# Kernel tuning notes

Hardware: AMD Instinct MI355X
Metric: run time of the kernel (lower is better)

Reference implementation:

```python
import jax, jax.numpy as jnp
import numpy as np

N, E, D = 50000, 1600000, 32
P = 2.0  # exponent self.p


def setup_inputs() -> dict:
    key = jax.random.key(0)
    k1, k2, k3 = jax.random.split(key, 3)
    X = jax.random.normal(k1, (N, D), dtype=jnp.float32)
    edge_index = jax.random.randint(k2, (2, E), 0, N)
    W = jax.random.normal(k3, (D, D), dtype=jnp.float32) / np.float32(np.sqrt(D))
    b = jnp.zeros((D,), dtype=jnp.float32)
    return {"X": X, "edge_index": edge_index, "W": W, "b": b}


def gcn_conv(X, edge_index, W, b, n):
    # PyG GCNConv: add self-loops, symmetric deg^-1/2 normalization,
    # aggregate messages from source col -> target row.
    src, dst = edge_index[0], edge_index[1]
    loops = jnp.arange(n)
    row = jnp.concatenate([dst, loops])  # targets
    col = jnp.concatenate([src, loops])  # sources
    deg = jax.ops.segment_sum(jnp.ones(row.shape, X.dtype), row, num_segments=n)
    dinv = jax.lax.rsqrt(jnp.maximum(deg, 1.0))  # deg >= 1 (self-loops)
    h = X @ W  # [N, D]
    msg = h[col] * (dinv[col] * dinv[row])[:, None]  # [E+N, D]
    return jax.ops.segment_sum(msg, row, num_segments=n) + b


def reference(X, edge_index, W, b):
    n = X.shape[0]
    h = jax.nn.relu(gcn_conv(X, edge_index, W, b, n))  # activation(conv(X, ei))
    src, dst = edge_index[0], edge_index[1]
    e = jnp.abs(h[src] - h[dst]) ** P  # [E, D] gather + pow
    s = jax.ops.segment_sum(e, src, num_segments=n)  # scatter-sum by source
    cnt = jax.ops.segment_sum(jnp.ones((e.shape[0],), h.dtype), src, num_segments=n)
    mean = s / jnp.maximum(cnt, 1.0)[:, None]  # scatter-mean finalize
    return jnp.tanh(mean)
```

## Files before the change

### kernel.cpp

```cpp
#include <hip/hip_runtime.h>

#define D 32
#define CSH 7
#define KMASK 127
#define PSH 23
#define PMASK ((1u << PSH) - 1u)
#define NBMAX 512

typedef unsigned int uint;

__device__ inline uint bf16rne(float f) {
    uint u = __float_as_uint(f);
    return (u + 0x7FFFu + ((u >> 16) & 1u)) >> 16;
}
__device__ inline float bf_lo(uint w) { return __uint_as_float(w << 16); }
__device__ inline float bf_hi(uint w) { return __uint_as_float(w & 0xFFFF0000u); }
__device__ inline uint bf_pack(float x, float y) { return bf16rne(x) | (bf16rne(y) << 16); }

__global__ void zero_kernel(int* __restrict__ p, int n) {
    int i = threadIdx.x;
    if (i < n) p[i] = 0;
}

__global__ void __launch_bounds__(1024)
coarse_scatter(const int* __restrict__ src, const int* __restrict__ dst,
               int* __restrict__ gCurD, int* __restrict__ gCurS,
               uint* __restrict__ coarseD, uint* __restrict__ coarseS,
               int E, int cap) {
    __shared__ uint stageD[4096], stageS[4096];
    __shared__ int hD[NBMAX], hS[NBMAX];
    __shared__ int preD[NBMAX], preS[NBMAX];
    __shared__ int offD[NBMAX + 1], offS[NBMAX + 1];
    __shared__ int baseD[NBMAX], baseS[NBMAX];
    int t = threadIdx.x;
    if (t < NBMAX) { hD[t] = 0; hS[t] = 0; }
    __syncthreads();
    int s[4], d[4], lpD[4], lpS[4];
    int j0 = blockIdx.x * 4096 + 4 * t;
    int nv = 0;
    if (j0 + 3 < E) {
        int4 s4 = *(const int4*)(src + j0);
        int4 d4 = *(const int4*)(dst + j0);
        s[0] = s4.x; s[1] = s4.y; s[2] = s4.z; s[3] = s4.w;
        d[0] = d4.x; d[1] = d4.y; d[2] = d4.z; d[3] = d4.w;
        nv = 4;
    } else {
        for (int u = 0; u < 4; ++u) {
            int j = j0 + u;
            if (j < E) { s[nv] = src[j]; d[nv] = dst[j]; ++nv; }
        }
    }
    for (int u = 0; u < nv; ++u) {
        lpD[u] = atomicAdd(&hD[d[u] >> CSH], 1);
        lpS[u] = atomicAdd(&hS[s[u] >> CSH], 1);
    }
    __syncthreads();
    {
        int l = t & (NBMAX - 1);
        int* h    = (t < NBMAX) ? hD : hS;
        int* pre  = (t < NBMAX) ? preD : preS;
        int* off  = (t < NBMAX) ? offD : offS;
        int* base = (t < NBMAX) ? baseD : baseS;
        int* gC   = (t < NBMAX) ? gCurD : gCurS;
        pre[l] = h[l];
        __syncthreads();
        for (int stp = 1; stp < NBMAX; stp <<= 1) {
            int x = (l >= stp) ? pre[l - stp] : 0;
            __syncthreads();
            pre[l] += x;
            __syncthreads();
        }
        off[l] = pre[l] - h[l];
        if (l == NBMAX - 1) off[NBMAX] = pre[l];
        if (h[l]) base[l] = atomicAdd(&gC[l], h[l]);
    }
    __syncthreads();
    for (int u = 0; u < nv; ++u) {
        stageD[offD[d[u] >> CSH] + lpD[u]] = ((uint)(d[u] & KMASK) << PSH) | (uint)s[u];
        stageS[offS[s[u] >> CSH] + lpS[u]] = ((uint)(s[u] & KMASK) << PSH) | (uint)d[u];
    }
    __syncthreads();
    int totD = offD[NBMAX];
    for (int j = t; j < totD; j += 1024) {
        int lo = 0, hi = NBMAX;
        while (hi - lo > 1) { int mid = (lo + hi) >> 1; if (offD[mid] <= j) lo = mid; else hi = mid; }
        int rel = baseD[lo] + (j - offD[lo]);
        if (rel < cap) coarseD[(size_t)lo * cap + rel] = stageD[j];
    }
    int totS = offS[NBMAX];
    for (int j = t; j < totS; j += 1024) {
        int lo = 0, hi = NBMAX;
        while (hi - lo > 1) { int mid = (lo + hi) >> 1; if (offS[mid] <= j) lo = mid; else hi = mid; }
        int rel = baseS[lo] + (j - offS[lo]);
        if (rel < cap) coarseS[(size_t)lo * cap + rel] = stageS[j];
    }
}

__global__ void deg_dinv_kernel(const uint* __restrict__ coarseD, const int* __restrict__ gCurD,
                                float* __restrict__ dinv, int N, int cap) {
    __shared__ int cnt[128];
    int b = blockIdx.x, t = threadIdx.x;
    if (t < 128) cnt[t] = 0;
    __syncthreads();
    size_t lo = (size_t)b * cap;
    int n = min(gCurD[b], cap - 512);
    int n4 = n >> 2;
    const uint4* c4 = (const uint4*)(coarseD + lo);
    for (int kk = t; kk < n4; kk += 1024) {
        uint4 e4 = c4[kk];
        atomicAdd(&cnt[e4.x >> PSH], 1);
        atomicAdd(&cnt[e4.y >> PSH], 1);
        atomicAdd(&cnt[e4.z >> PSH], 1);
        atomicAdd(&cnt[e4.w >> PSH], 1);
    }
    for (int kk = 4 * n4 + t; kk < n; kk += 1024)
        atomicAdd(&cnt[coarseD[lo + kk] >> PSH], 1);
    __syncthreads();
    int node = (b << CSH) + t;
    if (t < 128 && node < N) dinv[node] = rsqrtf((float)(cnt[t] + 1));
}

__global__ void matmul_scale_kernel(const float* __restrict__ X, const float* __restrict__ W,
                                    const float* __restrict__ dinv, uint* __restrict__ hs16,
                                    int N) {
    __shared__ float Wl[D * D];
    __shared__ float Xl[8 * D];
    int tid = threadIdx.x;
    for (int k = tid; k < D * D; k += 256) Wl[k] = W[k];
    int row0 = blockIdx.x * 8;
    int g = row0 * D + tid;
    Xl[tid] = (g < N * D) ? X[g] : 0.f;
    __syncthreads();
    int r = tid >> 5;
    int d = tid & 31;
    int row = row0 + r;
    float acc = 0.f;
    #pragma unroll
    for (int k = 0; k < D; ++k) acc += Xl[r * D + k] * Wl[k * D + d];
    if (row < N) acc *= dinv[row];
    float other = __shfl_xor(acc, 1);
    if (row < N && (d & 1) == 0)
        hs16[row * 16 + (d >> 1)] = bf_pack(acc, other);
}

__global__ void __launch_bounds__(1024)
conv_fused(const uint* __restrict__ coarseD, const int* __restrict__ gCurD,
           const uint* __restrict__ hs16, const float* __restrict__ bias,
           uint* __restrict__ h2_16, int N, int cap) {
    extern __shared__ uint adjL[];
    __shared__ int cnt[128];
    __shared__ int pre[128];
    __shared__ int rs[128];
    __shared__ int degL[128];
    int b = blockIdx.x;
    int t = threadIdx.x;
    int nodeLo = b << CSH;
    int nNodes = min(128, N - nodeLo);
    if (t < 128) cnt[t] = 0;
    __syncthreads();
    size_t lo = (size_t)b * cap;
    int n = min(gCurD[b], cap - 512);
    int n4 = n >> 2;
    const uint4* c4 = (const uint4*)(coarseD + lo);
    for (int kk = t; kk < n4; kk += 1024) {
        uint4 e4 = c4[kk];
        atomicAdd(&cnt[e4.x >> PSH], 1);
        atomicAdd(&cnt[e4.y >> PSH], 1);
        atomicAdd(&cnt[e4.z >> PSH], 1);
        atomicAdd(&cnt[e4.w >> PSH], 1);
    }
    for (int kk = 4 * n4 + t; kk < n; kk += 1024)
        atomicAdd(&cnt[coarseD[lo + kk] >> PSH], 1);
    __syncthreads();
    int mydeg = 0, mypad = 0;
    if (t < 128) { mydeg = cnt[t]; mypad = (mydeg + 3) & ~3; pre[t] = mypad; }
    __syncthreads();
    for (int off = 1; off < 128; off <<= 1) {
        int x = 0;
        if (t < 128 && t >= off) x = pre[t - off];
        __syncthreads();
        if (t < 128) pre[t] += x;
        __syncthreads();
    }
    if (t < 128) {
        rs[t] = pre[t] - mypad;
        degL[t] = mydeg;
        cnt[t] = pre[t] - mypad;
    }
    __syncthreads();
    for (int kk = t; kk < n; kk += 1024) {
        uint e = coarseD[lo + kk];
        int pos = atomicAdd(&cnt[e >> PSH], 1);
        if (pos < cap) adjL[pos] = e & PMASK;
    }
    __syncthreads();
    int wave = t >> 6, lane = t & 63;
    int p = lane & 15, slot = lane >> 4;
    for (int nl = wave; nl < nNodes; nl += 16) {
        int s = rs[nl];
        int e = s + degL[nl];
        float ax0 = 0.f, ay0 = 0.f, ax1 = 0.f, ay1 = 0.f;
        float ax2 = 0.f, ay2 = 0.f, ax3 = 0.f, ay3 = 0.f;
        int k = s;
        for (; k + 15 < e; k += 16) {
            uint4 iv = *(const uint4*)(adjL + k + slot * 4);
            uint w0 = hs16[iv.x * 16 + p];
            uint w1 = hs16[iv.y * 16 + p];
            uint w2 = hs16[iv.z * 16 + p];
            uint w3 = hs16[iv.w * 16 + p];
            ax0 += bf_lo(w0); ay0 += bf_hi(w0);
            ax1 += bf_lo(w1); ay1 += bf_hi(w1);
            ax2 += bf_lo(w2); ay2 += bf_hi(w2);
            ax3 += bf_lo(w3); ay3 += bf_hi(w3);
        }
        for (; k < e; k += 4) {
            int kk = k + slot;
            if (kk < e) {
                uint w = hs16[adjL[kk] * 16 + p];
                ax0 += bf_lo(w); ay0 += bf_hi(w);
            }
        }
        float accx = (ax0 + ax1) + (ax2 + ax3);
        float accy = (ay0 + ay1) + (ay2 + ay3);
        accx += __shfl_xor(accx, 16); accy += __shfl_xor(accy, 16);
        accx += __shfl_xor(accx, 32); accy += __shfl_xor(accy, 32);
        if (slot == 0) {
            int node = nodeLo + nl;
            uint wself = hs16[(size_t)node * 16 + p];
            float di = rsqrtf((float)(degL[nl] + 1));
            float vx = di * (accx + bf_lo(wself)) + bias[2 * p];
            float vy = di * (accy + bf_hi(wself)) + bias[2 * p + 1];
            h2_16[(size_t)node * 16 + p] = bf_pack(fmaxf(vx, 0.f), fmaxf(vy, 0.f));
        }
    }
}

__global__ void __launch_bounds__(1024)
pow_fused(const uint* __restrict__ coarseS, const int* __restrict__ gCurS,
          const uint* __restrict__ h2_16, float* __restrict__ out, int N, int cap) {
    extern __shared__ uint adjL[];
    __shared__ int cnt[128];
    __shared__ int pre[128];
    __shared__ int rs[128];
    __shared__ int degL[128];
    __shared__ uint self[128 * 16];
    int b = blockIdx.x;
    int t = threadIdx.x;
    int nodeLo = b << CSH;
    int nNodes = min(128, N - nodeLo);
    if (t < 128) cnt[t] = 0;
    for (int i = t; i < nNodes * 16; i += 1024)
        self[i] = h2_16[(size_t)(nodeLo + (i >> 4)) * 16 + (i & 15)];
    __syncthreads();
    size_t lo = (size_t)b * cap;
    int n = min(gCurS[b], cap - 512);
    int n4 = n >> 2;
    const uint4* c4 = (const uint4*)(coarseS + lo);
    for (int kk = t; kk < n4; kk += 1024) {
        uint4 e4 = c4[kk];
        atomicAdd(&cnt[e4.x >> PSH], 1);
        atomicAdd(&cnt[e4.y >> PSH], 1);
        atomicAdd(&cnt[e4.z >> PSH], 1);
        atomicAdd(&cnt[e4.w >> PSH], 1);
    }
    for (int kk = 4 * n4 + t; kk < n; kk += 1024)
        atomicAdd(&cnt[coarseS[lo + kk] >> PSH], 1);
    __syncthreads();
    int mydeg = 0, mypad = 0;
    if (t < 128) { mydeg = cnt[t]; mypad = (mydeg + 3) & ~3; pre[t] = mypad; }
    __syncthreads();
    for (int off = 1; off < 128; off <<= 1) {
        int x = 0;
        if (t < 128 && t >= off) x = pre[t - off];
        __syncthreads();
        if (t < 128) pre[t] += x;
        __syncthreads();
    }
    if (t < 128) {
        rs[t] = pre[t] - mypad;
        degL[t] = mydeg;
        cnt[t] = pre[t] - mypad;
    }
    __syncthreads();
    for (int kk = t; kk < n; kk += 1024) {
        uint e = coarseS[lo + kk];
        int pos = atomicAdd(&cnt[e >> PSH], 1);
        if (pos < cap) adjL[pos] = e & PMASK;
    }
    __syncthreads();
    int wave = t >> 6, lane = t & 63;
    int p = lane & 15, slot = lane >> 4;
    for (int nl = wave; nl < nNodes; nl += 16) {
        int s = rs[nl];
        int e = s + degL[nl];
        uint wh = self[nl * 16 + p];
        float hx = bf_lo(wh), hy = bf_hi(wh);
        float ax0 = 0.f, ay0 = 0.f, ax1 = 0.f, ay1 = 0.f;
        float ax2 = 0.f, ay2 = 0.f, ax3 = 0.f, ay3 = 0.f;
        int k = s;
        for (; k + 15 < e; k += 16) {
            uint4 iv = *(const uint4*)(adjL + k + slot * 4);
            uint w0 = h2_16[iv.x * 16 + p];
            uint w1 = h2_16[iv.y * 16 + p];
            uint w2 = h2_16[iv.z * 16 + p];
            uint w3 = h2_16[iv.w * 16 + p];
            float vx0 = hx - bf_lo(w0), vy0 = hy - bf_hi(w0);
            float vx1 = hx - bf_lo(w1), vy1 = hy - bf_hi(w1);
            float vx2 = hx - bf_lo(w2), vy2 = hy - bf_hi(w2);
            float vx3 = hx - bf_lo(w3), vy3 = hy - bf_hi(w3);
            ax0 += vx0 * vx0; ay0 += vy0 * vy0;
            ax1 += vx1 * vx1; ay1 += vy1 * vy1;
            ax2 += vx2 * vx2; ay2 += vy2 * vy2;
            ax3 += vx3 * vx3; ay3 += vy3 * vy3;
        }
        for (; k < e; k += 4) {
            int kk = k + slot;
            if (kk < e) {
                uint w = h2_16[adjL[kk] * 16 + p];
                float vx = hx - bf_lo(w), vy = hy - bf_hi(w);
                ax0 += vx * vx; ay0 += vy * vy;
            }
        }
        float accx = (ax0 + ax1) + (ax2 + ax3);
        float accy = (ay0 + ay1) + (ay2 + ay3);
        accx += __shfl_xor(accx, 16); accy += __shfl_xor(accy, 16);
        accx += __shfl_xor(accx, 32); accy += __shfl_xor(accy, 32);
        if (slot == 0) {
            float c = fmaxf((float)degL[nl], 1.f);
            float2 r;
            r.x = tanhf(accx / c);
            r.y = tanhf(accy / c);
            ((float2*)out)[(size_t)(nodeLo + nl) * 16 + p] = r;
        }
    }
}

__global__ void fb_count(const int* __restrict__ src, const int* __restrict__ dst,
                         int* __restrict__ degI, int* __restrict__ cntI, int E) {
    int j = blockIdx.x * blockDim.x + threadIdx.x;
    if (j < E) {
        atomicAdd(&degI[dst[j]], 1);
        atomicAdd(&cntI[src[j]], 1);
    }
}
__global__ void fb_dinv(const int* __restrict__ degI, float* __restrict__ dinv, int N) {
    int i = blockIdx.x * blockDim.x + threadIdx.x;
    if (i < N) dinv[i] = rsqrtf((float)(degI[i] + 1));
}
__global__ void fb_matmul(const float* __restrict__ X, const float* __restrict__ W,
                          const float* __restrict__ dinv, float* __restrict__ hs, int N) {
    __shared__ float Wl[D * D];
    __shared__ float Xl[8 * D];
    int tid = threadIdx.x;
    for (int k = tid; k < D * D; k += 256) Wl[k] = W[k];
    int row0 = blockIdx.x * 8;
    int g = row0 * D + tid;
    Xl[tid] = (g < N * D) ? X[g] : 0.f;
    __syncthreads();
    int r = tid >> 5;
    int d = tid & 31;
    int row = row0 + r;
    if (row < N) {
        float acc = 0.f;
        #pragma unroll
        for (int k = 0; k < D; ++k) acc += Xl[r * D + k] * Wl[k * D + d];
        hs[row * D + d] = acc * dinv[row];
    }
}
__global__ void fb_scatter_conv(const int* __restrict__ src, const int* __restrict__ dst,
                                const float* __restrict__ hs, float* __restrict__ S, int ED) {
    int idx = blockIdx.x * blockDim.x + threadIdx.x;
    if (idx < ED) {
        int j = idx >> 5, d = idx & 31;
        atomicAdd(&S[dst[j] * D + d], hs[src[j] * D + d]);
    }
}
__global__ void fb_h2(float* __restrict__ S, const float* __restrict__ hs,
                      const float* __restrict__ dinv, const float* __restrict__ b, int ND) {
    int idx = blockIdx.x * blockDim.x + threadIdx.x;
    if (idx < ND) {
        int i = idx >> 5, d = idx & 31;
        float v = dinv[i] * (S[idx] + hs[idx]) + b[d];
        S[idx] = fmaxf(v, 0.f);
    }
}
__global__ void fb_edge_pow(const int* __restrict__ src, const int* __restrict__ dst,
                            const float* __restrict__ h2, float* __restrict__ out, int ED) {
    int idx = blockIdx.x * blockDim.x + threadIdx.x;
    if (idx < ED) {
        int j = idx >> 5, d = idx & 31;
        float v = h2[src[j] * D + d] - h2[dst[j] * D + d];
        atomicAdd(&out[src[j] * D + d], v * v);
    }
}
__global__ void fb_finalize(float* __restrict__ out, const int* __restrict__ cntI, int ND) {
    int idx = blockIdx.x * blockDim.x + threadIdx.x;
    if (idx < ND) {
        int i = idx >> 5;
        float c = fmaxf((float)cntI[i], 1.f);
        out[idx] = tanhf(out[idx] / c);
    }
}

extern "C" void kernel_launch(void* const* d_in, const int* in_sizes, int n_in,
                              void* d_out, int out_size, void* d_ws, size_t ws_size,
                              hipStream_t stream) {
    const float* X  = (const float*)d_in[0];
    const int*   ei = (const int*)d_in[1];
    const float* W  = (const float*)d_in[2];
    const float* b  = (const float*)d_in[3];
    int N = in_sizes[0] / D;
    int E = in_sizes[1] / 2;
    const int* src = ei;
    const int* dst = ei + E;
    float* out = (float*)d_out;

    size_t ND = (size_t)N * D;
    size_t NH = (size_t)N * 16;
    int nb = (N + 127) >> CSH;
    int cap = ((E + nb - 1) / nb + 1024 + 15) & ~15;
    size_t capSz = (size_t)nb * cap;
    size_t ldsBytes = (size_t)cap * 4;

    uint* coarseD = (uint*)d_ws;
    uint* coarseS = coarseD + capSz;
    uint* hs16   = coarseS + capSz;
    uint* h2_16  = hs16 + NH;
    float* dinv = (float*)(h2_16 + NH);
    int* gCurD  = (int*)(dinv + N);
    int* gCurS  = gCurD + NBMAX;
    size_t need = (2 * capSz + 2 * NH + (size_t)N + 2 * NBMAX) * 4;

    if (ws_size >= need && nb <= NBMAX && N <= (1 << PSH) && capSz < (1u << 30)
        && ldsBytes <= 96 * 1024) {
        zero_kernel<<<1, 1024, 0, stream>>>(gCurD, 2 * NBMAX);
        int cgrid = (E + 4095) / 4096;
        coarse_scatter<<<cgrid, 1024, 0, stream>>>(src, dst, gCurD, gCurS,
                                                   coarseD, coarseS, E, cap);
        deg_dinv_kernel<<<nb, 1024, 0, stream>>>(coarseD, gCurD, dinv, N, cap);
        matmul_scale_kernel<<<(N + 7) / 8, 256, 0, stream>>>(X, W, dinv, hs16, N);
        conv_fused<<<nb, 1024, ldsBytes, stream>>>(coarseD, gCurD, hs16, b, h2_16, N, cap);
        pow_fused<<<nb, 1024, ldsBytes, stream>>>(coarseS, gCurS, h2_16, out, N, cap);
    } else {
        float* fhs  = (float*)d_ws;
        float* S    = fhs + ND;
        float* fdv  = S + ND;
        int*   fdeg = (int*)(fdv + N);
        int*   fcnt = fdeg + N;
        hipMemsetAsync(S, 0, ND * sizeof(float), stream);
        hipMemsetAsync(fdeg, 0, (size_t)2 * N * sizeof(int), stream);
        hipMemsetAsync(d_out, 0, ND * sizeof(float), stream);
        int EDi = E * D, NDi = (int)ND;
        fb_count<<<(E + 255) / 256, 256, 0, stream>>>(src, dst, fdeg, fcnt, E);
        fb_dinv<<<(N + 255) / 256, 256, 0, stream>>>(fdeg, fdv, N);
        fb_matmul<<<(N + 7) / 8, 256, 0, stream>>>(X, W, fdv, fhs, N);
        fb_scatter_conv<<<(EDi + 255) / 256, 256, 0, stream>>>(src, dst, fhs, S, EDi);
        fb_h2<<<(NDi + 255) / 256, 256, 0, stream>>>(S, fhs, fdv, b, NDi);
        fb_edge_pow<<<(EDi + 255) / 256, 256, 0, stream>>>(src, dst, S, out, EDi);
        fb_finalize<<<(NDi + 255) / 256, 256, 0, stream>>>(out, fcnt, NDi);
    }
}
```

Measured before the change: 95.23 us.

## Fuse degree counting with matmul and unroll gather loops to 32 edges

Merges the degree/dinv kernel and the X@W scale kernel into one per-bucket kernel that counts degrees in LDS and then computes the 128 rows of the bucket. This drops one launch and the dinv global array round-trip. It also adds a 32-edge unrolled gather loop in the conv and pow kernels so each lane has more loads in flight. The trade-off is that the matmul now runs on only about 391 blocks, each staging 16KB of X in LDS, which may reduce parallelism compared with the many small blocks it had before.

```diff
diff --git a/kernel.cpp b/kernel.cpp
--- a/kernel.cpp
+++ b/kernel.cpp
@@ -96,11 +96,21 @@
     }
 }
 
-__global__ void deg_dinv_kernel(const uint* __restrict__ coarseD, const int* __restrict__ gCurD,
-                                float* __restrict__ dinv, int N, int cap) {
+__global__ void __launch_bounds__(1024)
+matmul_deg_kernel(const float* __restrict__ X, const float* __restrict__ W,
+                  const uint* __restrict__ coarseD, const int* __restrict__ gCurD,
+                  uint* __restrict__ hs16, int N, int cap) {
+    __shared__ float Wl[D * D];
+    __shared__ float Xl[128 * D];
     __shared__ int cnt[128];
     int b = blockIdx.x, t = threadIdx.x;
+    int nodeLo = b << CSH;
     if (t < 128) cnt[t] = 0;
+    if (t < D * D) Wl[t] = W[t];
+    for (int i = t; i < 128 * D; i += 1024) {
+        int node = nodeLo + (i >> 5);
+        Xl[i] = (node < N) ? X[(size_t)node * D + (i & 31)] : 0.f;
+    }
     __syncthreads();
     size_t lo = (size_t)b * cap;
     int n = min(gCurD[b], cap - 512);
@@ -116,31 +126,19 @@
     for (int kk = 4 * n4 + t; kk < n; kk += 1024)
         atomicAdd(&cnt[coarseD[lo + kk] >> PSH], 1);
     __syncthreads();
-    int node = (b << CSH) + t;
-    if (t < 128 && node < N) dinv[node] = rsqrtf((float)(cnt[t] + 1));
-}
-
-__global__ void matmul_scale_kernel(const float* __restrict__ X, const float* __restrict__ W,
-                                    const float* __restrict__ dinv, uint* __restrict__ hs16,
-                                    int N) {
-    __shared__ float Wl[D * D];
-    __shared__ float Xl[8 * D];
-    int tid = threadIdx.x;
-    for (int k = tid; k < D * D; k += 256) Wl[k] = W[k];
-    int row0 = blockIdx.x * 8;
-    int g = row0 * D + tid;
-    Xl[tid] = (g < N * D) ? X[g] : 0.f;
-    __syncthreads();
-    int r = tid >> 5;
-    int d = tid & 31;
-    int row = row0 + r;
-    float acc = 0.f;
+    int c = t & 31;
     #pragma unroll
-    for (int k = 0; k < D; ++k) acc += Xl[r * D + k] * Wl[k * D + d];
-    if (row < N) acc *= dinv[row];
-    float other = __shfl_xor(acc, 1);
-    if (row < N && (d & 1) == 0)
-        hs16[row * 16 + (d >> 1)] = bf_pack(acc, other);
+    for (int pass = 0; pass < 4; ++pass) {
+        int r = pass * 32 + (t >> 5);
+        int node = nodeLo + r;
+        float acc = 0.f;
+        #pragma unroll
+        for (int k = 0; k < D; ++k) acc += Xl[r * D + k] * Wl[k * D + c];
+        acc *= rsqrtf((float)(cnt[r] + 1));
+        float other = __shfl_xor(acc, 1);
+        if (node < N && (c & 1) == 0)
+            hs16[(size_t)node * 16 + (c >> 1)] = bf_pack(acc, other);
+    }
 }
 
 __global__ void __launch_bounds__(1024)
@@ -202,6 +200,26 @@
         float ax0 = 0.f, ay0 = 0.f, ax1 = 0.f, ay1 = 0.f;
         float ax2 = 0.f, ay2 = 0.f, ax3 = 0.f, ay3 = 0.f;
         int k = s;
+        for (; k + 31 < e; k += 32) {
+            uint4 iv0 = *(const uint4*)(adjL + k + slot * 4);
+            uint4 iv1 = *(const uint4*)(adjL + k + 16 + slot * 4);
+            uint w0 = hs16[iv0.x * 16 + p];
+            uint w1 = hs16[iv0.y * 16 + p];
+            uint w2 = hs16[iv0.z * 16 + p];
+            uint w3 = hs16[iv0.w * 16 + p];
+            uint w4 = hs16[iv1.x * 16 + p];
+            uint w5 = hs16[iv1.y * 16 + p];
+            uint w6 = hs16[iv1.z * 16 + p];
+            uint w7 = hs16[iv1.w * 16 + p];
+            ax0 += bf_lo(w0); ay0 += bf_hi(w0);
+            ax1 += bf_lo(w1); ay1 += bf_hi(w1);
+            ax2 += bf_lo(w2); ay2 += bf_hi(w2);
+            ax3 += bf_lo(w3); ay3 += bf_hi(w3);
+            ax0 += bf_lo(w4); ay0 += bf_hi(w4);
+            ax1 += bf_lo(w5); ay1 += bf_hi(w5);
+            ax2 += bf_lo(w6); ay2 += bf_hi(w6);
+            ax3 += bf_lo(w7); ay3 += bf_hi(w7);
+        }
         for (; k + 15 < e; k += 16) {
             uint4 iv = *(const uint4*)(adjL + k + slot * 4);
             uint w0 = hs16[iv.x * 16 + p];
@@ -298,6 +316,34 @@
         float ax0 = 0.f, ay0 = 0.f, ax1 = 0.f, ay1 = 0.f;
         float ax2 = 0.f, ay2 = 0.f, ax3 = 0.f, ay3 = 0.f;
         int k = s;
+        for (; k + 31 < e; k += 32) {
+            uint4 iv0 = *(const uint4*)(adjL + k + slot * 4);
+            uint4 iv1 = *(const uint4*)(adjL + k + 16 + slot * 4);
+            uint w0 = h2_16[iv0.x * 16 + p];
+            uint w1 = h2_16[iv0.y * 16 + p];
+            uint w2 = h2_16[iv0.z * 16 + p];
+            uint w3 = h2_16[iv0.w * 16 + p];
+            uint w4 = h2_16[iv1.x * 16 + p];
+            uint w5 = h2_16[iv1.y * 16 + p];
+            uint w6 = h2_16[iv1.z * 16 + p];
+            uint w7 = h2_16[iv1.w * 16 + p];
+            float vx0 = hx - bf_lo(w0), vy0 = hy - bf_hi(w0);
+            float vx1 = hx - bf_lo(w1), vy1 = hy - bf_hi(w1);
+            float vx2 = hx - bf_lo(w2), vy2 = hy - bf_hi(w2);
+            float vx3 = hx - bf_lo(w3), vy3 = hy - bf_hi(w3);
+            ax0 += vx0 * vx0; ay0 += vy0 * vy0;
+            ax1 += vx1 * vx1; ay1 += vy1 * vy1;
+            ax2 += vx2 * vx2; ay2 += vy2 * vy2;
+            ax3 += vx3 * vx3; ay3 += vy3 * vy3;
+            float vx4 = hx - bf_lo(w4), vy4 = hy - bf_hi(w4);
+            float vx5 = hx - bf_lo(w5), vy5 = hy - bf_hi(w5);
+            float vx6 = hx - bf_lo(w6), vy6 = hy - bf_hi(w6);
+            float vx7 = hx - bf_lo(w7), vy7 = hy - bf_hi(w7);
+            ax0 += vx4 * vx4; ay0 += vy4 * vy4;
+            ax1 += vx5 * vx5; ay1 += vy5 * vy5;
+            ax2 += vx6 * vx6; ay2 += vy6 * vy6;
+            ax3 += vx7 * vx7; ay3 += vy7 * vy7;
+        }
         for (; k + 15 < e; k += 16) {
             uint4 iv = *(const uint4*)(adjL + k + slot * 4);
             uint w0 = h2_16[iv.x * 16 + p];
@@ -426,10 +472,9 @@
     uint* coarseS = coarseD + capSz;
     uint* hs16   = coarseS + capSz;
     uint* h2_16  = hs16 + NH;
-    float* dinv = (float*)(h2_16 + NH);
-    int* gCurD  = (int*)(dinv + N);
+    int* gCurD  = (int*)(h2_16 + NH);
     int* gCurS  = gCurD + NBMAX;
-    size_t need = (2 * capSz + 2 * NH + (size_t)N + 2 * NBMAX) * 4;
+    size_t need = (2 * capSz + 2 * NH + 2 * NBMAX) * 4;
 
     if (ws_size >= need && nb <= NBMAX && N <= (1 << PSH) && capSz < (1u << 30)
         && ldsBytes <= 96 * 1024) {
@@ -437,8 +482,7 @@
         int cgrid = (E + 4095) / 4096;
         coarse_scatter<<<cgrid, 1024, 0, stream>>>(src, dst, gCurD, gCurS,
                                                    coarseD, coarseS, E, cap);
-        deg_dinv_kernel<<<nb, 1024, 0, stream>>>(coarseD, gCurD, dinv, N, cap);
-        matmul_scale_kernel<<<(N + 7) / 8, 256, 0, stream>>>(X, W, dinv, hs16, N);
+        matmul_deg_kernel<<<nb, 1024, 0, stream>>>(X, W, coarseD, gCurD, hs16, N, cap);
         conv_fused<<<nb, 1024, ldsBytes, stream>>>(coarseD, gCurD, hs16, b, h2_16, N, cap);
         pow_fused<<<nb, 1024, ldsBytes, stream>>>(coarseS, gCurS, h2_16, out, N, cap);
     } else {
```

Result: faster. 91.88 us (-3.5%).
